# Kernel optimization log

Hardware: AMD Instinct MI355X
Metric: run time of the kernel (lower is better)

## Reference

```python
import jax, jax.numpy as jnp
import numpy as np

B, H, W, K, PAD = 1024, 28, 28, 3, 1


def conv3x3(x, w, b):
    out = jax.lax.conv_general_dilated(x, w, (1, 1), ((PAD, PAD), (PAD, PAD)),
                                       dimension_numbers=('NCHW', 'OIHW', 'NCHW'))
    return out + b[None, :, None, None]


def deform_conv2d(x, offset, w, b):
    # torchvision deform_conv2d semantics, stride=1, pad=1, dilation=1, groups=1
    Bn, Cin, Hh, Ww = x.shape
    Cout = w.shape[0]
    KK = K * K
    off = offset.reshape(Bn, KK, 2, Hh, Ww)
    dy, dx = off[:, :, 0], off[:, :, 1]                      # [B,KK,H,W]
    ky, kx = jnp.meshgrid(jnp.arange(K, dtype=x.dtype), jnp.arange(K, dtype=x.dtype), indexing='ij')
    py = dy + (jnp.arange(Hh, dtype=x.dtype) - PAD)[None, None, :, None] + ky.reshape(KK)[None, :, None, None]
    px = dx + (jnp.arange(Ww, dtype=x.dtype) - PAD)[None, None, None, :] + kx.reshape(KK)[None, :, None, None]
    y0 = jnp.floor(py); x0 = jnp.floor(px)
    wy1 = py - y0; wy0 = 1.0 - wy1
    wx1 = px - x0; wx0 = 1.0 - wx1
    xf = x.reshape(Bn, Cin, Hh * Ww)

    def gather(yi, xi):
        valid = (yi >= 0) & (yi < Hh) & (xi >= 0) & (xi < Ww)
        yc = jnp.clip(yi, 0, Hh - 1).astype(jnp.int32)
        xc = jnp.clip(xi, 0, Ww - 1).astype(jnp.int32)
        idx = (yc * Ww + xc).reshape(Bn, -1)                 # [B, KK*H*W]
        g = jnp.take_along_axis(xf, jnp.broadcast_to(idx[:, None, :], (Bn, Cin, idx.shape[1])), axis=2)
        return g.reshape(Bn, Cin, KK, Hh, Ww) * valid.astype(x.dtype)[:, None]

    sampled = (gather(y0, x0) * (wy0 * wx0)[:, None]
               + gather(y0, x0 + 1) * (wy0 * wx1)[:, None]
               + gather(y0 + 1, x0) * (wy1 * wx0)[:, None]
               + gather(y0 + 1, x0 + 1) * (wy1 * wx1)[:, None])  # [B,Cin,KK,H,W]
    out = jnp.einsum('bkhw,ok->bohw', sampled.reshape(Bn, Cin * KK, Hh, Ww),
                     w.reshape(Cout, Cin * KK))
    return out + b[None, :, None, None]


def adaptive_avg_pool_14(x):
    Bn, C, Hh, Ww = x.shape
    f = Hh // 14
    return x.reshape(Bn, C, 14, f, 14, f).mean(axis=(3, 5))


def setup_inputs() -> dict:
    key = jax.random.key(0)
    ks = jax.random.split(key, 14)
    d = {}
    d['x'] = jax.random.normal(ks[0], (B, 1, H, W), dtype=jnp.float32)
    # offset conv 1: Conv2d(1, 18, 3, pad=1)
    d['ow1'] = jax.random.normal(ks[1], (18, 1, 3, 3), dtype=jnp.float32) * 0.1
    d['ob1'] = jnp.zeros((18,), jnp.float32)
    d['w1'] = jax.random.normal(ks[2], (32, 1, 3, 3), dtype=jnp.float32) * 0.01
    d['b1'] = jnp.zeros((32,), jnp.float32)
    # offset conv 2: Conv2d(32, 18, 3, pad=1)
    d['ow2'] = jax.random.normal(ks[3], (18, 32, 3, 3), dtype=jnp.float32) * 0.05
    d['ob2'] = jnp.zeros((18,), jnp.float32)
    d['w2'] = jax.random.normal(ks[4], (64, 32, 3, 3), dtype=jnp.float32) * 0.01
    d['b2'] = jnp.zeros((64,), jnp.float32)
    d['fw1'] = jax.random.normal(ks[5], (128, 64 * 14 * 14), dtype=jnp.float32) * 0.01
    d['fb1'] = jnp.zeros((128,), jnp.float32)
    d['fw2'] = jax.random.normal(ks[6], (10, 128), dtype=jnp.float32) * 0.05
    d['fb2'] = jnp.zeros((10,), jnp.float32)
    return d


def reference(x, ow1, ob1, w1, b1, ow2, ob2, w2, b2, fw1, fb1, fw2, fb2):
    # block1 + relu + pool 28->14
    h = deform_conv2d(x, conv3x3(x, ow1, ob1), w1, b1)
    h = adaptive_avg_pool_14(jax.nn.relu(h))
    # block2 + relu + pool 14->14 (identity)
    h = deform_conv2d(h, conv3x3(h, ow2, ob2), w2, b2)
    h = adaptive_avg_pool_14(jax.nn.relu(h))
    h = h.reshape(h.shape[0], -1)
    # classifier (ExcitationDropout is identity in eval mode)
    h = jax.nn.relu(h @ fw1.T + fb1)
    return h @ fw2.T + fb2
```

## Files before the change

kernel.cpp:

```cpp
#include <hip/hip_runtime.h>

#define NB 1024
#define TOTAL1 (NB*196)
#define SP 208

#define WS_H1   0
#define WS_H2   6422528
#define WS_PART 19267584
#define WS_W1T  23461888
#define WS_OW1T 23462176
#define WS_W2T  23462338
#define WS_OW2T 23480770

__global__ __launch_bounds__(256) void prep(const float* __restrict__ w1,
                                            const float* __restrict__ ow1,
                                            const float* __restrict__ w2,
                                            const float* __restrict__ ow2,
                                            float* __restrict__ ws) {
  int i = blockIdx.x * 256 + threadIdx.x;
  if (i < 288)   { int co = i / 9,  kk = i % 9;   ws[WS_W1T  + kk * 32 + co] = w1[i]; }
  if (i < 162)   { int c  = i / 9,  j  = i % 9;   ws[WS_OW1T + j  * 18 + c ] = ow1[i]; }
  if (i < 18432) { int co = i / 288, k = i % 288; ws[WS_W2T  + k  * 64 + co] = w2[i]; }
  if (i < 5184)  { int c  = i / 288, k = i % 288; ws[WS_OW2T + k  * 18 + c ] = ow2[i]; }
}

__global__ __launch_bounds__(256, 2) void stage1(const float* __restrict__ x,
                                                 const float* __restrict__ ob1,
                                                 const float* __restrict__ b1,
                                                 const float* __restrict__ ws,
                                                 float* __restrict__ h1) {
  __shared__ float ximg[3 * 784];
  const float* __restrict__ w1t  = ws + WS_W1T;
  const float* __restrict__ ow1t = ws + WS_OW1T;
  int tid = threadIdx.x;
  int g0 = blockIdx.x * 256;
  int bfirst = g0 / 196;
  for (int idx = tid; idx < 3 * 784; idx += 256) {
    int img = idx / 784;
    int b = bfirst + img;
    ximg[idx] = (b < NB) ? x[b * 784 + (idx - img * 784)] : 0.f;
  }
  __syncthreads();
  int g = g0 + tid;
  if (g >= TOTAL1) return;
  int b = g / 196, p = g - b * 196;
  const float* im = ximg + (b - bfirst) * 784;
  int oy = p / 14, ox = p - (p / 14) * 14;

  float pooled[32];
#pragma unroll
  for (int co = 0; co < 32; ++co) pooled[co] = 0.f;

  for (int sub = 0; sub < 4; ++sub) {
    int y  = 2 * oy + (sub >> 1);
    int ix = 2 * ox + (sub & 1);
    float patch[9];
#pragma unroll
    for (int j = 0; j < 9; ++j) {
      int yy = y + j / 3 - 1, xc = ix + j % 3 - 1;
      bool ok = (yy >= 0) & (yy < 28) & (xc >= 0) & (xc < 28);
      patch[j] = ok ? im[yy * 28 + xc] : 0.f;
    }
    float off[18];
#pragma unroll
    for (int c = 0; c < 18; ++c) off[c] = ob1[c];
#pragma unroll
    for (int j = 0; j < 9; ++j) {
      float v = patch[j];
#pragma unroll
      for (int c = 0; c < 18; ++c) off[c] = fmaf(v, ow1t[j * 18 + c], off[c]);
    }
    float a[32];
#pragma unroll
    for (int co = 0; co < 32; ++co) a[co] = b1[co];
#pragma unroll
    for (int kk = 0; kk < 9; ++kk) {
      float py = (float)(y - 1 + kk / 3) + off[2 * kk];
      float px = (float)(ix - 1 + kk % 3) + off[2 * kk + 1];
      float y0f = floorf(py), x0f = floorf(px);
      float wy1 = py - y0f, wx1 = px - x0f;
      float wy0 = 1.f - wy1, wx0 = 1.f - wx1;
      int y0 = (int)y0f, x0 = (int)x0f;
      int y1 = y0 + 1, x1 = x0 + 1;
      bool vy0 = (y0 >= 0) & (y0 < 28), vy1 = (y1 >= 0) & (y1 < 28);
      bool vx0 = (x0 >= 0) & (x0 < 28), vx1 = (x1 >= 0) & (x1 < 28);
      float W00 = (vy0 & vx0) ? wy0 * wx0 : 0.f;
      float W01 = (vy0 & vx1) ? wy0 * wx1 : 0.f;
      float W10 = (vy1 & vx0) ? wy1 * wx0 : 0.f;
      float W11 = (vy1 & vx1) ? wy1 * wx1 : 0.f;
      int yc0 = min(max(y0, 0), 27), yc1 = min(max(y1, 0), 27);
      int xc0 = min(max(x0, 0), 27), xc1 = min(max(x1, 0), 27);
      float s = im[yc0 * 28 + xc0] * W00 + im[yc0 * 28 + xc1] * W01 +
                im[yc1 * 28 + xc0] * W10 + im[yc1 * 28 + xc1] * W11;
#pragma unroll
      for (int co = 0; co < 32; ++co) a[co] = fmaf(s, w1t[kk * 32 + co], a[co]);
    }
#pragma unroll
    for (int co = 0; co < 32; ++co) pooled[co] += fmaxf(a[co], 0.f);
  }
#pragma unroll
  for (int co = 0; co < 32; ++co) h1[b * 6272 + co * 196 + p] = pooled[co] * 0.25f;
}

__global__ __launch_bounds__(256, 2) void stage2(const float* __restrict__ h1,
                                                 const float* __restrict__ ob2,
                                                 const float* __restrict__ b2,
                                                 const float* __restrict__ ws,
                                                 float* __restrict__ h2) {
  __shared__ float imgT[196 * 32];
  __shared__ float offs[18 * SP];
  __shared__ float Sbuf[32 * SP];
  const float* __restrict__ w2t  = ws + WS_W2T;
  const float* __restrict__ ow2t = ws + WS_OW2T;
  int tid = threadIdx.x;
  int b = blockIdx.x;

  for (int e = tid; e < 6272; e += 256) {
    int ci = e / 196, p = e - ci * 196;
    imgT[p * 32 + ((ci + 4 * p) & 31)] = h1[b * 6272 + e];
  }

  int pp = tid;
  int spy = pp / 14, spx = pp - (pp / 14) * 14;

  int oc  = tid % 18;
  int opg = tid / 18;
  int op0 = opg * 16;
  bool oact = (tid < 234);
  float oacc[16];
#pragma unroll
  for (int i = 0; i < 16; ++i) oacc[i] = 0.f;

  for (int j = 0; j < 9; ++j) {
    __syncthreads();
    if (pp < SP) {
      if (pp < 196) {
        int yy = spy + j / 3 - 1, xx = spx + j % 3 - 1;
        bool ok = (yy >= 0) & (yy < 14) & (xx >= 0) & (xx < 14);
        int idx = ok ? (yy * 14 + xx) : 0;
        const float* src = imgT + idx * 32;
        int rot = (4 * idx) & 31;
#pragma unroll
        for (int cg = 0; cg < 8; ++cg) {
          float4 v;
          if (ok) v = *(const float4*)(src + ((cg * 4 + rot) & 31));
          else    v = make_float4(0.f, 0.f, 0.f, 0.f);
          Sbuf[(cg * 4 + 0) * SP + pp] = v.x;
          Sbuf[(cg * 4 + 1) * SP + pp] = v.y;
          Sbuf[(cg * 4 + 2) * SP + pp] = v.z;
          Sbuf[(cg * 4 + 3) * SP + pp] = v.w;
        }
      } else {
#pragma unroll
        for (int ci2 = 0; ci2 < 32; ++ci2) Sbuf[ci2 * SP + pp] = 0.f;
      }
    }
    __syncthreads();
    if (oact) {
      float wv[32];
#pragma unroll
      for (int ci2 = 0; ci2 < 32; ++ci2) wv[ci2] = ow2t[(ci2 * 9 + j) * 18 + oc];
      for (int ci2 = 0; ci2 < 32; ++ci2) {
        const float* srow = Sbuf + ci2 * SP + op0;
        float w = wv[ci2];
#pragma unroll
        for (int t = 0; t < 4; ++t) {
          float4 s = *(const float4*)(srow + 4 * t);
          oacc[4 * t + 0] = fmaf(w, s.x, oacc[4 * t + 0]);
          oacc[4 * t + 1] = fmaf(w, s.y, oacc[4 * t + 1]);
          oacc[4 * t + 2] = fmaf(w, s.z, oacc[4 * t + 2]);
          oacc[4 * t + 3] = fmaf(w, s.w, oacc[4 * t + 3]);
        }
      }
    }
  }
  __syncthreads();
  if (oact) {
    float bo = ob2[oc];
#pragma unroll
    for (int i = 0; i < 16; ++i) offs[oc * SP + op0 + i] = oacc[i] + bo;
  }

  int cog = tid & 15, pg = tid >> 4;
  int co0 = cog * 4;
  int p0 = pg * 16;
  bool gact = (pg < 13);
  float acc[4][16];
  {
    float4 bb = *(const float4*)(b2 + co0);
    float bj[4] = {bb.x, bb.y, bb.z, bb.w};
#pragma unroll
    for (int j = 0; j < 4; ++j)
#pragma unroll
      for (int i = 0; i < 16; ++i) acc[j][i] = bj[j];
  }

  for (int kk = 0; kk < 9; ++kk) {
    __syncthreads();
    if (pp < SP) {
      if (pp < 196) {
        float dyv = offs[(2 * kk) * SP + pp];
        float dxv = offs[(2 * kk + 1) * SP + pp];
        float pyv = (float)(spy - 1 + kk / 3) + dyv;
        float pxv = (float)(spx - 1 + kk % 3) + dxv;
        float y0f = floorf(pyv), x0f = floorf(pxv);
        float wy1 = pyv - y0f, wx1 = pxv - x0f;
        float wy0 = 1.f - wy1, wx0 = 1.f - wx1;
        int y0 = (int)y0f, x0 = (int)x0f;
        int y1 = y0 + 1, x1 = x0 + 1;
        bool vy0 = (y0 >= 0) & (y0 < 14), vy1 = (y1 >= 0) & (y1 < 14);
        bool vx0 = (x0 >= 0) & (x0 < 14), vx1 = (x1 >= 0) & (x1 < 14);
        float W00 = (vy0 & vx0) ? wy0 * wx0 : 0.f;
        float W01 = (vy0 & vx1) ? wy0 * wx1 : 0.f;
        float W10 = (vy1 & vx0) ? wy1 * wx0 : 0.f;
        float W11 = (vy1 & vx1) ? wy1 * wx1 : 0.f;
        int yc0 = min(max(y0, 0), 13), yc1 = min(max(y1, 0), 13);
        int xc0 = min(max(x0, 0), 13), xc1 = min(max(x1, 0), 13);
        int i00 = yc0 * 14 + xc0, i01 = yc0 * 14 + xc1;
        int i10 = yc1 * 14 + xc0, i11 = yc1 * 14 + xc1;
        const float* s00 = imgT + i00 * 32; int r00 = (4 * i00) & 31;
        const float* s01 = imgT + i01 * 32; int r01 = (4 * i01) & 31;
        const float* s10 = imgT + i10 * 32; int r10 = (4 * i10) & 31;
        const float* s11 = imgT + i11 * 32; int r11 = (4 * i11) & 31;
#pragma unroll
        for (int cg = 0; cg < 8; ++cg) {
          float4 a0 = *(const float4*)(s00 + ((cg * 4 + r00) & 31));
          float4 a1 = *(const float4*)(s01 + ((cg * 4 + r01) & 31));
          float4 a2 = *(const float4*)(s10 + ((cg * 4 + r10) & 31));
          float4 a3 = *(const float4*)(s11 + ((cg * 4 + r11) & 31));
          Sbuf[(cg * 4 + 0) * SP + pp] = fmaf(W00, a0.x, fmaf(W01, a1.x, fmaf(W10, a2.x, W11 * a3.x)));
          Sbuf[(cg * 4 + 1) * SP + pp] = fmaf(W00, a0.y, fmaf(W01, a1.y, fmaf(W10, a2.y, W11 * a3.y)));
          Sbuf[(cg * 4 + 2) * SP + pp] = fmaf(W00, a0.z, fmaf(W01, a1.z, fmaf(W10, a2.z, W11 * a3.z)));
          Sbuf[(cg * 4 + 3) * SP + pp] = fmaf(W00, a0.w, fmaf(W01, a1.w, fmaf(W10, a2.w, W11 * a3.w)));
        }
      } else {
#pragma unroll
        for (int ci2 = 0; ci2 < 32; ++ci2) Sbuf[ci2 * SP + pp] = 0.f;
      }
    }
    __syncthreads();
    if (gact) {
      for (int cb = 0; cb < 32; cb += 8) {
        float4 w[8];
#pragma unroll
        for (int u = 0; u < 8; ++u)
          w[u] = *(const float4*)(w2t + ((cb + u) * 9 + kk) * 64 + co0);
#pragma unroll
        for (int u = 0; u < 8; ++u) {
          const float* srow = Sbuf + (cb + u) * SP + p0;
          float4 s0 = *(const float4*)(srow);
          float4 s1 = *(const float4*)(srow + 4);
          float4 s2 = *(const float4*)(srow + 8);
          float4 s3 = *(const float4*)(srow + 12);
          float sv[16] = {s0.x, s0.y, s0.z, s0.w, s1.x, s1.y, s1.z, s1.w,
                          s2.x, s2.y, s2.z, s2.w, s3.x, s3.y, s3.z, s3.w};
          float wj[4] = {w[u].x, w[u].y, w[u].z, w[u].w};
#pragma unroll
          for (int j = 0; j < 4; ++j)
#pragma unroll
            for (int i = 0; i < 16; ++i)
              acc[j][i] = fmaf(wj[j], sv[i], acc[j][i]);
        }
      }
    }
  }

  if (gact) {
    float* __restrict__ orow = h2 + b * 12544 + co0 * 196 + p0;
#pragma unroll
    for (int j = 0; j < 4; ++j) {
#pragma unroll
      for (int t = 0; t < 4; ++t) {
        if (p0 + 4 * t < 196) {
          float4 v;
          v.x = fmaxf(acc[j][4 * t + 0], 0.f);
          v.y = fmaxf(acc[j][4 * t + 1], 0.f);
          v.z = fmaxf(acc[j][4 * t + 2], 0.f);
          v.w = fmaxf(acc[j][4 * t + 3], 0.f);
          *(float4*)(orow + j * 196 + 4 * t) = v;
        }
      }
    }
  }
}

__global__ __launch_bounds__(256, 2) void fc1(const float* __restrict__ h2,
                                              const float* __restrict__ fw1,
                                              float* __restrict__ part) {
  __shared__ float a_s[56 * 72];
  __shared__ float b_s[56 * 132];
  int tid = threadIdx.x;
  int rb = (blockIdx.x & 15) * 64;
  int ks = blockIdx.x >> 4;
  int kbase = ks * 392;
  int c0 = (tid & 31) * 4;
  int r0 = (tid >> 5) * 8;

  float acc[8][4];
#pragma unroll
  for (int i = 0; i < 8; ++i)
#pragma unroll
    for (int j = 0; j < 4; ++j) acc[i][j] = 0.f;

  for (int ch = 0; ch < 7; ++ch) {
    int kb = kbase + ch * 56;
    __syncthreads();
#pragma unroll
    for (int t = 0; t < 14; ++t) {
      int idx = t * 256 + tid;
      int r = idx / 56, k = idx - r * 56;
      a_s[k * 72 + r] = h2[(rb + r) * 12544 + kb + k];
    }
#pragma unroll
    for (int t = 0; t < 28; ++t) {
      int idx = t * 256 + tid;
      int c = idx / 56, k = idx - c * 56;
      b_s[k * 132 + c] = fw1[c * 12544 + kb + k];
    }
    __syncthreads();
    for (int k = 0; k < 56; ++k) {
      float4 bv = *(const float4*)&b_s[k * 132 + c0];
      float4 av0 = *(const float4*)&a_s[k * 72 + r0];
      float4 av1 = *(const float4*)&a_s[k * 72 + r0 + 4];
      float av[8] = {av0.x, av0.y, av0.z, av0.w, av1.x, av1.y, av1.z, av1.w};
      float bj[4] = {bv.x, bv.y, bv.z, bv.w};
#pragma unroll
      for (int i = 0; i < 8; ++i)
#pragma unroll
        for (int j = 0; j < 4; ++j) acc[i][j] = fmaf(av[i], bj[j], acc[i][j]);
    }
  }
#pragma unroll
  for (int i = 0; i < 8; ++i) {
    int r = rb + r0 + i;
#pragma unroll
    for (int j = 0; j < 4; ++j)
      part[(ks * 1024 + r) * 128 + c0 + j] = acc[i][j];
  }
}

__global__ __launch_bounds__(128) void fcfinal(const float* __restrict__ part,
                                               const float* __restrict__ fb1,
                                               const float* __restrict__ fw2,
                                               const float* __restrict__ fb2,
                                               float* __restrict__ out) {
  __shared__ float tbuf[128];
  int b = blockIdx.x, c = threadIdx.x;
  float s = fb1[c];
  for (int ks = 0; ks < 32; ++ks) s += part[(ks * 1024 + b) * 128 + c];
  tbuf[c] = fmaxf(s, 0.f);
  __syncthreads();
  if (c < 10) {
    float v = fb2[c];
#pragma unroll
    for (int k = 0; k < 128; ++k) v = fmaf(tbuf[k], fw2[c * 128 + k], v);
    out[b * 10 + c] = v;
  }
}

extern "C" void kernel_launch(void* const* d_in, const int* in_sizes, int n_in,
                              void* d_out, int out_size, void* d_ws, size_t ws_size,
                              hipStream_t stream) {
  const float* x   = (const float*)d_in[0];
  const float* ow1 = (const float*)d_in[1];
  const float* ob1 = (const float*)d_in[2];
  const float* w1  = (const float*)d_in[3];
  const float* b1  = (const float*)d_in[4];
  const float* ow2 = (const float*)d_in[5];
  const float* ob2 = (const float*)d_in[6];
  const float* w2  = (const float*)d_in[7];
  const float* b2  = (const float*)d_in[8];
  const float* fw1 = (const float*)d_in[9];
  const float* fb1 = (const float*)d_in[10];
  const float* fw2 = (const float*)d_in[11];
  const float* fb2 = (const float*)d_in[12];
  float* ws  = (float*)d_ws;
  float* out = (float*)d_out;

  prep<<<72, 256, 0, stream>>>(w1, ow1, w2, ow2, ws);
  stage1<<<784, 256, 0, stream>>>(x, ob1, b1, ws, ws + WS_H1);
  stage2<<<NB, 256, 0, stream>>>(ws + WS_H1, ob2, b2, ws, ws + WS_H2);
  fc1<<<512, 256, 0, stream>>>(ws + WS_H2, fw1, ws + WS_PART);
  fcfinal<<<1024, 128, 0, stream>>>(ws + WS_PART, fb1, fw2, fb2, out);
}
```

Before: 385.7 us.

## Shrink stage2 shared memory to fit three blocks per CU

```diff
diff --git a/kernel.cpp b/kernel.cpp
--- a/kernel.cpp
+++ b/kernel.cpp
@@ -2,7 +2,7 @@
 
 #define NB 1024
 #define TOTAL1 (NB*196)
-#define SP 208
+#define SPS 200
 
 #define WS_H1   0
 #define WS_H2   6422528
@@ -102,14 +102,14 @@
   for (int co = 0; co < 32; ++co) h1[b * 6272 + co * 196 + p] = pooled[co] * 0.25f;
 }
 
-__global__ __launch_bounds__(256, 2) void stage2(const float* __restrict__ h1,
+__global__ __launch_bounds__(256, 3) void stage2(const float* __restrict__ h1,
                                                  const float* __restrict__ ob2,
                                                  const float* __restrict__ b2,
                                                  const float* __restrict__ ws,
                                                  float* __restrict__ h2) {
   __shared__ float imgT[196 * 32];
-  __shared__ float offs[18 * SP];
-  __shared__ float Sbuf[32 * SP];
+  __shared__ float Sbuf[32 * SPS + 8];
+  __shared__ float offT[2 * 208];
   const float* __restrict__ w2t  = ws + WS_W2T;
   const float* __restrict__ ow2t = ws + WS_OW2T;
   int tid = threadIdx.x;
@@ -133,27 +133,25 @@
 
   for (int j = 0; j < 9; ++j) {
     __syncthreads();
-    if (pp < SP) {
-      if (pp < 196) {
-        int yy = spy + j / 3 - 1, xx = spx + j % 3 - 1;
-        bool ok = (yy >= 0) & (yy < 14) & (xx >= 0) & (xx < 14);
-        int idx = ok ? (yy * 14 + xx) : 0;
-        const float* src = imgT + idx * 32;
-        int rot = (4 * idx) & 31;
-#pragma unroll
-        for (int cg = 0; cg < 8; ++cg) {
-          float4 v;
-          if (ok) v = *(const float4*)(src + ((cg * 4 + rot) & 31));
-          else    v = make_float4(0.f, 0.f, 0.f, 0.f);
-          Sbuf[(cg * 4 + 0) * SP + pp] = v.x;
-          Sbuf[(cg * 4 + 1) * SP + pp] = v.y;
-          Sbuf[(cg * 4 + 2) * SP + pp] = v.z;
-          Sbuf[(cg * 4 + 3) * SP + pp] = v.w;
-        }
-      } else {
-#pragma unroll
-        for (int ci2 = 0; ci2 < 32; ++ci2) Sbuf[ci2 * SP + pp] = 0.f;
-      }
+    if (pp < 196) {
+      int yy = spy + j / 3 - 1, xx = spx + j % 3 - 1;
+      bool ok = (yy >= 0) & (yy < 14) & (xx >= 0) & (xx < 14);
+      int idx = ok ? (yy * 14 + xx) : 0;
+      const float* src = imgT + idx * 32;
+      int rot = (4 * idx) & 31;
+#pragma unroll
+      for (int cg = 0; cg < 8; ++cg) {
+        float4 v;
+        if (ok) v = *(const float4*)(src + ((cg * 4 + rot) & 31));
+        else    v = make_float4(0.f, 0.f, 0.f, 0.f);
+        Sbuf[(cg * 4 + 0) * SPS + pp] = v.x;
+        Sbuf[(cg * 4 + 1) * SPS + pp] = v.y;
+        Sbuf[(cg * 4 + 2) * SPS + pp] = v.z;
+        Sbuf[(cg * 4 + 3) * SPS + pp] = v.w;
+      }
+    } else if (pp < SPS) {
+#pragma unroll
+      for (int ci2 = 0; ci2 < 32; ++ci2) Sbuf[ci2 * SPS + pp] = 0.f;
     }
     __syncthreads();
     if (oact) {
@@ -161,7 +159,7 @@
 #pragma unroll
       for (int ci2 = 0; ci2 < 32; ++ci2) wv[ci2] = ow2t[(ci2 * 9 + j) * 18 + oc];
       for (int ci2 = 0; ci2 < 32; ++ci2) {
-        const float* srow = Sbuf + ci2 * SP + op0;
+        const float* srow = Sbuf + ci2 * SPS + op0;
         float w = wv[ci2];
 #pragma unroll
         for (int t = 0; t < 4; ++t) {
@@ -173,12 +171,6 @@
         }
       }
     }
-  }
-  __syncthreads();
-  if (oact) {
-    float bo = ob2[oc];
-#pragma unroll
-    for (int i = 0; i < 16; ++i) offs[oc * SP + op0 + i] = oacc[i] + bo;
   }
 
   int cog = tid & 15, pg = tid >> 4;
@@ -190,64 +182,69 @@
     float4 bb = *(const float4*)(b2 + co0);
     float bj[4] = {bb.x, bb.y, bb.z, bb.w};
 #pragma unroll
-    for (int j = 0; j < 4; ++j)
-#pragma unroll
-      for (int i = 0; i < 16; ++i) acc[j][i] = bj[j];
-  }
+    for (int jj = 0; jj < 4; ++jj)
+#pragma unroll
+      for (int i = 0; i < 16; ++i) acc[jj][i] = bj[jj];
+  }
+  float myob = oact ? ob2[oc] : 0.f;
 
   for (int kk = 0; kk < 9; ++kk) {
     __syncthreads();
-    if (pp < SP) {
-      if (pp < 196) {
-        float dyv = offs[(2 * kk) * SP + pp];
-        float dxv = offs[(2 * kk + 1) * SP + pp];
-        float pyv = (float)(spy - 1 + kk / 3) + dyv;
-        float pxv = (float)(spx - 1 + kk % 3) + dxv;
-        float y0f = floorf(pyv), x0f = floorf(pxv);
-        float wy1 = pyv - y0f, wx1 = pxv - x0f;
-        float wy0 = 1.f - wy1, wx0 = 1.f - wx1;
-        int y0 = (int)y0f, x0 = (int)x0f;
-        int y1 = y0 + 1, x1 = x0 + 1;
-        bool vy0 = (y0 >= 0) & (y0 < 14), vy1 = (y1 >= 0) & (y1 < 14);
-        bool vx0 = (x0 >= 0) & (x0 < 14), vx1 = (x1 >= 0) & (x1 < 14);
-        float W00 = (vy0 & vx0) ? wy0 * wx0 : 0.f;
-        float W01 = (vy0 & vx1) ? wy0 * wx1 : 0.f;
-        float W10 = (vy1 & vx0) ? wy1 * wx0 : 0.f;
-        float W11 = (vy1 & vx1) ? wy1 * wx1 : 0.f;
-        int yc0 = min(max(y0, 0), 13), yc1 = min(max(y1, 0), 13);
-        int xc0 = min(max(x0, 0), 13), xc1 = min(max(x1, 0), 13);
-        int i00 = yc0 * 14 + xc0, i01 = yc0 * 14 + xc1;
-        int i10 = yc1 * 14 + xc0, i11 = yc1 * 14 + xc1;
-        const float* s00 = imgT + i00 * 32; int r00 = (4 * i00) & 31;
-        const float* s01 = imgT + i01 * 32; int r01 = (4 * i01) & 31;
-        const float* s10 = imgT + i10 * 32; int r10 = (4 * i10) & 31;
-        const float* s11 = imgT + i11 * 32; int r11 = (4 * i11) & 31;
-#pragma unroll
-        for (int cg = 0; cg < 8; ++cg) {
-          float4 a0 = *(const float4*)(s00 + ((cg * 4 + r00) & 31));
-          float4 a1 = *(const float4*)(s01 + ((cg * 4 + r01) & 31));
-          float4 a2 = *(const float4*)(s10 + ((cg * 4 + r10) & 31));
-          float4 a3 = *(const float4*)(s11 + ((cg * 4 + r11) & 31));
-          Sbuf[(cg * 4 + 0) * SP + pp] = fmaf(W00, a0.x, fmaf(W01, a1.x, fmaf(W10, a2.x, W11 * a3.x)));
-          Sbuf[(cg * 4 + 1) * SP + pp] = fmaf(W00, a0.y, fmaf(W01, a1.y, fmaf(W10, a2.y, W11 * a3.y)));
-          Sbuf[(cg * 4 + 2) * SP + pp] = fmaf(W00, a0.z, fmaf(W01, a1.z, fmaf(W10, a2.z, W11 * a3.z)));
-          Sbuf[(cg * 4 + 3) * SP + pp] = fmaf(W00, a0.w, fmaf(W01, a1.w, fmaf(W10, a2.w, W11 * a3.w)));
-        }
-      } else {
-#pragma unroll
-        for (int ci2 = 0; ci2 < 32; ++ci2) Sbuf[ci2 * SP + pp] = 0.f;
-      }
+    if (oact && (oc >> 1) == kk) {
+      float* dst = offT + (oc & 1) * 208 + op0;
+#pragma unroll
+      for (int i = 0; i < 16; ++i) dst[i] = oacc[i] + myob;
+    }
+    __syncthreads();
+    if (pp < 196) {
+      float dyv = offT[pp];
+      float dxv = offT[208 + pp];
+      float pyv = (float)(spy - 1 + kk / 3) + dyv;
+      float pxv = (float)(spx - 1 + kk % 3) + dxv;
+      float y0f = floorf(pyv), x0f = floorf(pxv);
+      float wy1 = pyv - y0f, wx1 = pxv - x0f;
+      float wy0 = 1.f - wy1, wx0 = 1.f - wx1;
+      int y0 = (int)y0f, x0 = (int)x0f;
+      int y1 = y0 + 1, x1 = x0 + 1;
+      bool vy0 = (y0 >= 0) & (y0 < 14), vy1 = (y1 >= 0) & (y1 < 14);
+      bool vx0 = (x0 >= 0) & (x0 < 14), vx1 = (x1 >= 0) & (x1 < 14);
+      float W00 = (vy0 & vx0) ? wy0 * wx0 : 0.f;
+      float W01 = (vy0 & vx1) ? wy0 * wx1 : 0.f;
+      float W10 = (vy1 & vx0) ? wy1 * wx0 : 0.f;
+      float W11 = (vy1 & vx1) ? wy1 * wx1 : 0.f;
+      int yc0 = min(max(y0, 0), 13), yc1 = min(max(y1, 0), 13);
+      int xc0 = min(max(x0, 0), 13), xc1 = min(max(x1, 0), 13);
+      int i00 = yc0 * 14 + xc0, i01 = yc0 * 14 + xc1;
+      int i10 = yc1 * 14 + xc0, i11 = yc1 * 14 + xc1;
+      const float* s00 = imgT + i00 * 32; int r00 = (4 * i00) & 31;
+      const float* s01 = imgT + i01 * 32; int r01 = (4 * i01) & 31;
+      const float* s10 = imgT + i10 * 32; int r10 = (4 * i10) & 31;
+      const float* s11 = imgT + i11 * 32; int r11 = (4 * i11) & 31;
+#pragma unroll
+      for (int cg = 0; cg < 8; ++cg) {
+        float4 a0 = *(const float4*)(s00 + ((cg * 4 + r00) & 31));
+        float4 a1 = *(const float4*)(s01 + ((cg * 4 + r01) & 31));
+        float4 a2 = *(const float4*)(s10 + ((cg * 4 + r10) & 31));
+        float4 a3 = *(const float4*)(s11 + ((cg * 4 + r11) & 31));
+        Sbuf[(cg * 4 + 0) * SPS + pp] = fmaf(W00, a0.x, fmaf(W01, a1.x, fmaf(W10, a2.x, W11 * a3.x)));
+        Sbuf[(cg * 4 + 1) * SPS + pp] = fmaf(W00, a0.y, fmaf(W01, a1.y, fmaf(W10, a2.y, W11 * a3.y)));
+        Sbuf[(cg * 4 + 2) * SPS + pp] = fmaf(W00, a0.z, fmaf(W01, a1.z, fmaf(W10, a2.z, W11 * a3.z)));
+        Sbuf[(cg * 4 + 3) * SPS + pp] = fmaf(W00, a0.w, fmaf(W01, a1.w, fmaf(W10, a2.w, W11 * a3.w)));
+      }
+    } else if (pp < SPS) {
+#pragma unroll
+      for (int ci2 = 0; ci2 < 32; ++ci2) Sbuf[ci2 * SPS + pp] = 0.f;
     }
     __syncthreads();
     if (gact) {
-      for (int cb = 0; cb < 32; cb += 8) {
-        float4 w[8];
-#pragma unroll
-        for (int u = 0; u < 8; ++u)
+      for (int cb = 0; cb < 32; cb += 4) {
+        float4 w[4];
+#pragma unroll
+        for (int u = 0; u < 4; ++u)
           w[u] = *(const float4*)(w2t + ((cb + u) * 9 + kk) * 64 + co0);
 #pragma unroll
-        for (int u = 0; u < 8; ++u) {
-          const float* srow = Sbuf + (cb + u) * SP + p0;
+        for (int u = 0; u < 4; ++u) {
+          const float* srow = Sbuf + (cb + u) * SPS + p0;
           float4 s0 = *(const float4*)(srow);
           float4 s1 = *(const float4*)(srow + 4);
           float4 s2 = *(const float4*)(srow + 8);
@@ -256,10 +253,10 @@
                           s2.x, s2.y, s2.z, s2.w, s3.x, s3.y, s3.z, s3.w};
           float wj[4] = {w[u].x, w[u].y, w[u].z, w[u].w};
 #pragma unroll
-          for (int j = 0; j < 4; ++j)
+          for (int jj = 0; jj < 4; ++jj)
 #pragma unroll
             for (int i = 0; i < 16; ++i)
-              acc[j][i] = fmaf(wj[j], sv[i], acc[j][i]);
+              acc[jj][i] = fmaf(wj[jj], sv[i], acc[jj][i]);
         }
       }
     }
@@ -268,16 +265,16 @@
   if (gact) {
     float* __restrict__ orow = h2 + b * 12544 + co0 * 196 + p0;
 #pragma unroll
-    for (int j = 0; j < 4; ++j) {
+    for (int jj = 0; jj < 4; ++jj) {
 #pragma unroll
       for (int t = 0; t < 4; ++t) {
         if (p0 + 4 * t < 196) {
           float4 v;
-          v.x = fmaxf(acc[j][4 * t + 0], 0.f);
-          v.y = fmaxf(acc[j][4 * t + 1], 0.f);
-          v.z = fmaxf(acc[j][4 * t + 2], 0.f);
-          v.w = fmaxf(acc[j][4 * t + 3], 0.f);
-          *(float4*)(orow + j * 196 + 4 * t) = v;
+          v.x = fmaxf(acc[jj][4 * t + 0], 0.f);
+          v.y = fmaxf(acc[jj][4 * t + 1], 0.f);
+          v.z = fmaxf(acc[jj][4 * t + 2], 0.f);
+          v.w = fmaxf(acc[jj][4 * t + 3], 0.f);
+          *(float4*)(orow + jj * 196 + 4 * t) = v;
         }
       }
     }
```

Result: no change. 383.2 us (-0.6%).
